# Optimization experiments

Hardware: AMD Instinct MI355X
Metric: run time of the kernel (lower is better)

## Reference

```python
import jax, jax.numpy as jnp
import numpy as np

MAX_DEG = 6


def neighbor_lookup(atoms, edges, maskvalue, include_self):
    # atoms: (B, A, F), edges: (B, A, D) with -1 padding
    B, A, F = atoms.shape
    D = edges.shape[-1]
    mask = edges >= 0
    idx = jnp.where(mask, edges, 0).reshape(B, A * D)
    g = jnp.take_along_axis(atoms, idx[:, :, None], axis=1).reshape(B, A, D, F)
    g = jnp.where(mask[..., None], g, maskvalue)
    if include_self:
        g = jnp.concatenate([atoms[:, :, None, :], g], axis=2)  # (B,A,D+1,F)
    return g


def graph_conv(atoms, bonds, edges, W, b):
    # W: (MAX_DEG, F_in+BF, C), b: (MAX_DEG, C)
    deg = (edges >= 0).sum(-1)  # (B, A)
    summed_atoms = neighbor_lookup(atoms, edges, 0.0, True).sum(2)  # self + neighbors
    summed_bonds = bonds.sum(2)
    feats = jnp.concatenate([summed_atoms, summed_bonds], axis=-1)
    out = jnp.zeros(feats.shape[:2] + (W.shape[-1],), feats.dtype)
    for d in range(MAX_DEG):  # small fixed loop over degrees
        h = jax.nn.relu(feats @ W[d] + b[d])
        out = out + jnp.where((deg == d)[..., None], h, 0.0)
    return out


def graph_pool(atoms, edges):
    g = neighbor_lookup(atoms, edges, -jnp.inf, True)  # self included -> finite max
    return g.max(axis=2)


def graph_output(atoms, bonds, edges, Wo, bo):
    deg = (edges >= 0).sum(-1)
    feats = jnp.concatenate([atoms, bonds.sum(2)], axis=-1)
    out = jax.nn.softmax(feats @ Wo + bo, axis=-1)
    mask = (deg != 0)[..., None]  # zero out padded atoms
    return jnp.where(mask, out, 0.0).sum(axis=1)  # (B, hid)


def setup_inputs():
    key = jax.random.key(0)
    ks = jax.random.split(key, 16)
    B, A, D = 4096, 64, 6
    AF, BF, H = 37, 6, 128
    s = lambda k, sh: (jax.random.normal(k, sh, jnp.float32) * 0.05)
    return {
        "atoms": jax.random.normal(ks[0], (B, A, AF), jnp.float32),
        "bonds": jax.random.normal(ks[1], (B, A, D, BF), jnp.float32),
        "edges": jax.random.randint(ks[2], (B, A, D), -1, A),
        "W1": s(ks[3], (MAX_DEG, AF + BF, H)),
        "b1": s(ks[4], (MAX_DEG, H)),
        "W2": s(ks[5], (MAX_DEG, H + BF, H)),
        "b2": s(ks[6], (MAX_DEG, H)),
        "Wo": s(ks[7], (H + BF, H)),
        "bo": s(ks[8], (H,)),
        "Wm1": s(ks[9], (H, H // 2)),
        "bm1": s(ks[10], (H // 2,)),
        "Wm2": s(ks[11], (H // 2, H // 4)),
        "bm2": s(ks[12], (H // 4,)),
        "Wm3": s(ks[13], (H // 4, 1)),
        "bm3": s(ks[14], (1,)),
    }


def reference(atoms, bonds, edges, W1, b1, W2, b2, Wo, bo, Wm1, bm1, Wm2, bm2, Wm3, bm3):
    x = graph_conv(atoms, bonds, edges, W1, b1)
    x = graph_pool(x, edges)
    x = graph_conv(x, bonds, edges, W2, b2)
    x = graph_pool(x, edges)
    fp = graph_output(x, bonds, edges, Wo, bo)
    h = jax.nn.relu(fp @ Wm1 + bm1)
    h = jax.nn.relu(h @ Wm2 + bm2)
    out = (h @ Wm3 + bm3).squeeze()  # (B,)
    return out
```

## Files before the change

kernel.cpp:

```cpp
#include <hip/hip_runtime.h>
#include <math.h>


__device__ __forceinline__ float4 max4(float4 a, float4 b) {
  return make_float4(fmaxf(a.x, b.x), fmaxf(a.y, b.y), fmaxf(a.z, b.z), fmaxf(a.w, b.w));
}

__device__ __forceinline__ float4 nbr_max(const float4* sx4, const int* se, int a, int c4) {
  float4 m = sx4[a * 32 + c4];
#pragma unroll
  for (int d = 0; d < 6; ++d) {
    int e = se[a * 6 + d];
    if (e >= 0) m = max4(m, sx4[e * 32 + c4]);
  }
  return m;
}

__device__ __forceinline__ float4 nbr_sum(const float4* sx4, const int* se, int a, int c4) {
  float4 s = sx4[a * 32 + c4];
#pragma unroll
  for (int d = 0; d < 6; ++d) {
    int e = se[a * 6 + d];
    if (e >= 0) {
      float4 v = sx4[e * 32 + c4];
      s.x += v.x; s.y += v.y; s.z += v.z; s.w += v.w;
    }
  }
  return s;
}

__device__ __forceinline__ float4 nbr_wmax(const float4* sx4, const int* se, const int* sdeg,
                                           int a, int c4) {
  float4 m = make_float4(0.f, 0.f, 0.f, 0.f);
  if (sdeg[a] < 6) m = max4(m, sx4[a * 32 + c4]);
#pragma unroll
  for (int d = 0; d < 6; ++d) {
    int e = se[a * 6 + d];
    if (e >= 0 && sdeg[e] < 6) m = max4(m, sx4[e * 32 + c4]);
  }
  return m;
}

__global__ __launch_bounds__(512, 8) void qsar_fused(
    const float* __restrict__ atoms, const float* __restrict__ bonds,
    const int* __restrict__ edges,
    const float* __restrict__ W1, const float* __restrict__ b1,
    const float* __restrict__ W2, const float* __restrict__ b2,
    const float* __restrict__ Wo, const float* __restrict__ bo,
    const float* __restrict__ Wm1, const float* __restrict__ bm1,
    const float* __restrict__ Wm2, const float* __restrict__ bm2,
    const float* __restrict__ Wm3, const float* __restrict__ bm3,
    float* __restrict__ out)
{
  const int b    = blockIdx.x;
  const int tid  = threadIdx.x;
  const int hid  = tid >> 5;
  const int hl   = tid & 31;

  __shared__ float s_x[64 * 128];
  __shared__ float s_sa[608];
  __shared__ float s_bsum[64 * 8];
  __shared__ int   s_edges[64 * 6];
  __shared__ int   s_deg[64];
  __shared__ int   s_work[64];
  __shared__ int   s_perm[64];
  __shared__ float s_rsum[64];
  __shared__ int   s_nwork, s_na, s_nz;

  float4* sx4  = reinterpret_cast<float4*>(s_x);
  float*  s_fp = s_sa;
  float*  s_h1 = s_sa + 512;
  float*  s_h2 = s_sa + 576;

  {
    const int* ge = edges + (size_t)b * (64 * 6);
    for (int i = tid; i < 64 * 6; i += 512) s_edges[i] = ge[i];
    const float* gb = bonds + (size_t)b * (64 * 36);
    for (int i = tid; i < 64 * 6; i += 512) {
      int a = i / 6, f = i - a * 6;
      float s = 0.f;
#pragma unroll
      for (int d = 0; d < 6; ++d) s += gb[a * 36 + d * 6 + f];
      s_bsum[a * 8 + f] = s;
    }
#pragma unroll
    for (int j = 0; j < 4; ++j) sx4[tid + j * 512] = make_float4(0.f, 0.f, 0.f, 0.f);
    if (tid == 0) { s_nwork = 0; s_na = 0; s_nz = 0; }
  }
  __syncthreads();

  if (tid < 64) {
    int dcnt = 0;
#pragma unroll
    for (int d = 0; d < 6; ++d) dcnt += (s_edges[tid * 6 + d] >= 0) ? 1 : 0;
    s_deg[tid] = dcnt;
    if (dcnt < 6) { int p = atomicAdd(&s_nwork, 1); s_work[p] = tid; }
  }
  __syncthreads();

  if (tid < 64) {
    int nzf = (s_deg[tid] < 6) ? 1 : 0;
#pragma unroll
    for (int d = 0; d < 6; ++d) {
      int e = s_edges[tid * 6 + d];
      if (e >= 0 && s_deg[e] < 6) nzf = 1;
    }
    if (nzf) { int p = atomicAdd(&s_na, 1); s_perm[p] = tid; }
    else     { int p = atomicAdd(&s_nz, 1); s_perm[63 - p] = tid; }
  }

  {
    const int nw = s_nwork;
    const float* ga = atoms + (size_t)b * (64 * 37);
    const int c0 = hl * 4;
    for (int cb = 0; cb < nw; cb += 16) {
      const int cnt = (nw - cb < 16) ? (nw - cb) : 16;
      for (int i = tid; i < cnt * 37; i += 512) {
        int wi = i / 37, k = i - wi * 37;
        int a = s_work[cb + wi];
        float f = ga[a * 37 + k];
#pragma unroll
        for (int d = 0; d < 6; ++d) {
          int e = s_edges[a * 6 + d];
          if (e >= 0) f += ga[e * 37 + k];
        }
        s_sa[wi * 38 + k] = f;
      }
      __syncthreads();
      for (int w = hid; w < cnt; w += 16) {
        const int a = s_work[cb + w];
        const int d = s_deg[a];
        const float4* wdf4 = reinterpret_cast<const float4*>(W1 + d * (43 * 128));
        float4 acc = *reinterpret_cast<const float4*>(&b1[d * 128 + c0]);
#pragma unroll 4
        for (int k = 0; k < 37; ++k) {
          const float ff = s_sa[w * 38 + k];
          const float4 w4 = wdf4[k * 32 + hl];
          acc.x = fmaf(ff, w4.x, acc.x); acc.y = fmaf(ff, w4.y, acc.y);
          acc.z = fmaf(ff, w4.z, acc.z); acc.w = fmaf(ff, w4.w, acc.w);
        }
#pragma unroll
        for (int kk = 0; kk < 6; ++kk) {
          const float ff = s_bsum[a * 8 + kk];
          const float4 w4 = wdf4[(37 + kk) * 32 + hl];
          acc.x = fmaf(ff, w4.x, acc.x); acc.y = fmaf(ff, w4.y, acc.y);
          acc.z = fmaf(ff, w4.z, acc.z); acc.w = fmaf(ff, w4.w, acc.w);
        }
        *reinterpret_cast<float4*>(&s_x[a * 128 + c0]) =
            make_float4(fmaxf(acc.x, 0.f), fmaxf(acc.y, 0.f),
                        fmaxf(acc.z, 0.f), fmaxf(acc.w, 0.f));
      }
      __syncthreads();
    }
  }
  __syncthreads();

  {
    float4 v0 = nbr_max(sx4, s_edges, (tid + 0 * 512) >> 5, tid & 31);
    float4 v1 = nbr_max(sx4, s_edges, (tid + 1 * 512) >> 5, tid & 31);
    float4 v2 = nbr_max(sx4, s_edges, (tid + 2 * 512) >> 5, tid & 31);
    float4 v3 = nbr_max(sx4, s_edges, (tid + 3 * 512) >> 5, tid & 31);
    __syncthreads();
    sx4[tid + 0 * 512] = v0; sx4[tid + 1 * 512] = v1;
    sx4[tid + 2 * 512] = v2; sx4[tid + 3 * 512] = v3;
  }
  __syncthreads();

  {
    const float4 z = make_float4(0.f, 0.f, 0.f, 0.f);
    float4 v0 = z, v1 = z, v2 = z, v3 = z;
    if (s_deg[(tid + 0 * 512) >> 5] < 6) v0 = nbr_sum(sx4, s_edges, (tid + 0 * 512) >> 5, tid & 31);
    if (s_deg[(tid + 1 * 512) >> 5] < 6) v1 = nbr_sum(sx4, s_edges, (tid + 1 * 512) >> 5, tid & 31);
    if (s_deg[(tid + 2 * 512) >> 5] < 6) v2 = nbr_sum(sx4, s_edges, (tid + 2 * 512) >> 5, tid & 31);
    if (s_deg[(tid + 3 * 512) >> 5] < 6) v3 = nbr_sum(sx4, s_edges, (tid + 3 * 512) >> 5, tid & 31);
    __syncthreads();
    if (s_deg[(tid + 0 * 512) >> 5] < 6) sx4[tid + 0 * 512] = v0;
    if (s_deg[(tid + 1 * 512) >> 5] < 6) sx4[tid + 1 * 512] = v1;
    if (s_deg[(tid + 2 * 512) >> 5] < 6) sx4[tid + 2 * 512] = v2;
    if (s_deg[(tid + 3 * 512) >> 5] < 6) sx4[tid + 3 * 512] = v3;
  }
  __syncthreads();

  {
    const int nw = s_nwork;
    const int c0 = hl * 4;
    for (int w = hid; w < nw; w += 16) {
      const int a = s_work[w];
      const int d = s_deg[a];
      const float4* wdf4 = reinterpret_cast<const float4*>(W2 + d * (134 * 128));
      float4 acc = *reinterpret_cast<const float4*>(&b2[d * 128 + c0]);
#pragma unroll 4
      for (int k = 0; k < 128; ++k) {
        const float ff = s_x[a * 128 + k];
        const float4 w4 = wdf4[k * 32 + hl];
        acc.x = fmaf(ff, w4.x, acc.x); acc.y = fmaf(ff, w4.y, acc.y);
        acc.z = fmaf(ff, w4.z, acc.z); acc.w = fmaf(ff, w4.w, acc.w);
      }
#pragma unroll
      for (int kk = 0; kk < 6; ++kk) {
        const float ff = s_bsum[a * 8 + kk];
        const float4 w4 = wdf4[(128 + kk) * 32 + hl];
        acc.x = fmaf(ff, w4.x, acc.x); acc.y = fmaf(ff, w4.y, acc.y);
        acc.z = fmaf(ff, w4.z, acc.z); acc.w = fmaf(ff, w4.w, acc.w);
      }
      *reinterpret_cast<float4*>(&s_x[a * 128 + c0]) =
          make_float4(fmaxf(acc.x, 0.f), fmaxf(acc.y, 0.f),
                      fmaxf(acc.z, 0.f), fmaxf(acc.w, 0.f));
    }
  }
  __syncthreads();

  {
    float4 v0 = nbr_wmax(sx4, s_edges, s_deg, (tid + 0 * 512) >> 5, tid & 31);
    float4 v1 = nbr_wmax(sx4, s_edges, s_deg, (tid + 1 * 512) >> 5, tid & 31);
    float4 v2 = nbr_wmax(sx4, s_edges, s_deg, (tid + 2 * 512) >> 5, tid & 31);
    float4 v3 = nbr_wmax(sx4, s_edges, s_deg, (tid + 3 * 512) >> 5, tid & 31);
    __syncthreads();
    sx4[tid + 0 * 512] = v0; sx4[tid + 1 * 512] = v1;
    sx4[tid + 2 * 512] = v2; sx4[tid + 3 * 512] = v3;
  }
  __syncthreads();

  {
    const int c0 = hl * 4;
    const int na = s_na;
    const int sl = hid * 4;
    const int at0 = s_perm[sl + 0], at1 = s_perm[sl + 1];
    const int at2 = s_perm[sl + 2], at3 = s_perm[sl + 3];
    float a00 = 0.f, a01 = 0.f, a02 = 0.f, a03 = 0.f;
    float a10 = 0.f, a11 = 0.f, a12 = 0.f, a13 = 0.f;
    float a20 = 0.f, a21 = 0.f, a22 = 0.f, a23 = 0.f;
    float a30 = 0.f, a31 = 0.f, a32 = 0.f, a33 = 0.f;
    const float4* Wof4 = reinterpret_cast<const float4*>(Wo);
    if (sl < na) {
#pragma unroll 4
      for (int k = 0; k < 128; ++k) {
        const float4 w4 = Wof4[k * 32 + hl];
        const float f0 = s_x[at0 * 128 + k], f1 = s_x[at1 * 128 + k];
        const float f2 = s_x[at2 * 128 + k], f3 = s_x[at3 * 128 + k];
        a00 = fmaf(f0, w4.x, a00); a01 = fmaf(f0, w4.y, a01);
        a02 = fmaf(f0, w4.z, a02); a03 = fmaf(f0, w4.w, a03);
        a10 = fmaf(f1, w4.x, a10); a11 = fmaf(f1, w4.y, a11);
        a12 = fmaf(f1, w4.z, a12); a13 = fmaf(f1, w4.w, a13);
        a20 = fmaf(f2, w4.x, a20); a21 = fmaf(f2, w4.y, a21);
        a22 = fmaf(f2, w4.z, a22); a23 = fmaf(f2, w4.w, a23);
        a30 = fmaf(f3, w4.x, a30); a31 = fmaf(f3, w4.y, a31);
        a32 = fmaf(f3, w4.z, a32); a33 = fmaf(f3, w4.w, a33);
      }
    }
#pragma unroll
    for (int kk = 0; kk < 6; ++kk) {
      const float4 w4 = Wof4[(128 + kk) * 32 + hl];
      const float f0 = s_bsum[at0 * 8 + kk], f1 = s_bsum[at1 * 8 + kk];
      const float f2 = s_bsum[at2 * 8 + kk], f3 = s_bsum[at3 * 8 + kk];
      a00 = fmaf(f0, w4.x, a00); a01 = fmaf(f0, w4.y, a01);
      a02 = fmaf(f0, w4.z, a02); a03 = fmaf(f0, w4.w, a03);
      a10 = fmaf(f1, w4.x, a10); a11 = fmaf(f1, w4.y, a11);
      a12 = fmaf(f1, w4.z, a12); a13 = fmaf(f1, w4.w, a13);
      a20 = fmaf(f2, w4.x, a20); a21 = fmaf(f2, w4.y, a21);
      a22 = fmaf(f2, w4.z, a22); a23 = fmaf(f2, w4.w, a23);
      a30 = fmaf(f3, w4.x, a30); a31 = fmaf(f3, w4.y, a31);
      a32 = fmaf(f3, w4.z, a32); a33 = fmaf(f3, w4.w, a33);
    }
    const float4 bo4 = *reinterpret_cast<const float4*>(bo + c0);
    *reinterpret_cast<float4*>(&s_x[at0 * 128 + c0]) =
        make_float4(a00 + bo4.x, a01 + bo4.y, a02 + bo4.z, a03 + bo4.w);
    *reinterpret_cast<float4*>(&s_x[at1 * 128 + c0]) =
        make_float4(a10 + bo4.x, a11 + bo4.y, a12 + bo4.z, a13 + bo4.w);
    *reinterpret_cast<float4*>(&s_x[at2 * 128 + c0]) =
        make_float4(a20 + bo4.x, a21 + bo4.y, a22 + bo4.z, a23 + bo4.w);
    *reinterpret_cast<float4*>(&s_x[at3 * 128 + c0]) =
        make_float4(a30 + bo4.x, a31 + bo4.y, a32 + bo4.z, a33 + bo4.w);
  }
  __syncthreads();

  {
    const int a = tid >> 3, q = tid & 7;
    float* base = &s_x[a * 128 + q * 16];
    const float4 v0 = *reinterpret_cast<const float4*>(base + ((0 + tid) & 3) * 4);
    const float4 v1 = *reinterpret_cast<const float4*>(base + ((1 + tid) & 3) * 4);
    const float4 v2 = *reinterpret_cast<const float4*>(base + ((2 + tid) & 3) * 4);
    const float4 v3 = *reinterpret_cast<const float4*>(base + ((3 + tid) & 3) * 4);
    float mx = fmaxf(fmaxf(fmaxf(v0.x, v0.y), fmaxf(v0.z, v0.w)),
                     fmaxf(fmaxf(v1.x, v1.y), fmaxf(v1.z, v1.w)));
    mx = fmaxf(mx, fmaxf(fmaxf(fmaxf(v2.x, v2.y), fmaxf(v2.z, v2.w)),
                         fmaxf(fmaxf(v3.x, v3.y), fmaxf(v3.z, v3.w))));
    mx = fmaxf(mx, __shfl_xor(mx, 1));
    mx = fmaxf(mx, __shfl_xor(mx, 2));
    mx = fmaxf(mx, __shfl_xor(mx, 4));
    float4 e0, e1, e2, e3;
    e0.x = __expf(v0.x - mx); e0.y = __expf(v0.y - mx); e0.z = __expf(v0.z - mx); e0.w = __expf(v0.w - mx);
    e1.x = __expf(v1.x - mx); e1.y = __expf(v1.y - mx); e1.z = __expf(v1.z - mx); e1.w = __expf(v1.w - mx);
    e2.x = __expf(v2.x - mx); e2.y = __expf(v2.y - mx); e2.z = __expf(v2.z - mx); e2.w = __expf(v2.w - mx);
    e3.x = __expf(v3.x - mx); e3.y = __expf(v3.y - mx); e3.z = __expf(v3.z - mx); e3.w = __expf(v3.w - mx);
    float sm = e0.x + e0.y + e0.z + e0.w;
    sm += e1.x + e1.y + e1.z + e1.w;
    sm += e2.x + e2.y + e2.z + e2.w;
    sm += e3.x + e3.y + e3.z + e3.w;
    *reinterpret_cast<float4*>(base + ((0 + tid) & 3) * 4) = e0;
    *reinterpret_cast<float4*>(base + ((1 + tid) & 3) * 4) = e1;
    *reinterpret_cast<float4*>(base + ((2 + tid) & 3) * 4) = e2;
    *reinterpret_cast<float4*>(base + ((3 + tid) & 3) * 4) = e3;
    sm += __shfl_xor(sm, 1);
    sm += __shfl_xor(sm, 2);
    sm += __shfl_xor(sm, 4);
    if (q == 0) s_rsum[a] = (s_deg[a] != 0) ? (1.f / sm) : 0.f;
  }
  __syncthreads();

  {
    const int c = tid & 127, quarter = tid >> 7;
    float s = 0.f;
    for (int a2 = quarter * 16; a2 < quarter * 16 + 16; ++a2)
      s = fmaf(s_x[a2 * 128 + c], s_rsum[a2], s);
    s_fp[quarter * 128 + c] = s;
  }
  __syncthreads();
  if (tid < 128) s_fp[tid] += s_fp[128 + tid] + s_fp[256 + tid] + s_fp[384 + tid];
  __syncthreads();

  if (tid < 64) {
    float acc = bm1[tid];
    for (int k = 0; k < 128; ++k) acc = fmaf(s_fp[k], Wm1[k * 64 + tid], acc);
    s_h1[tid] = fmaxf(acc, 0.f);
  }
  __syncthreads();
  if (tid < 32) {
    float acc = bm2[tid];
    for (int k = 0; k < 64; ++k) acc = fmaf(s_h1[k], Wm2[k * 32 + tid], acc);
    s_h2[tid] = fmaxf(acc, 0.f);
  }
  __syncthreads();
  if (tid < 64) {
    float p = (tid < 32) ? s_h2[tid] * Wm3[tid] : 0.f;
#pragma unroll
    for (int off = 32; off > 0; off >>= 1) p += __shfl_xor(p, off);
    if (tid == 0) out[b] = p + bm3[0];
  }
}

extern "C" void kernel_launch(void* const* d_in, const int* in_sizes, int n_in,
                              void* d_out, int out_size, void* d_ws, size_t ws_size,
                              hipStream_t stream) {
  const float* atoms = (const float*)d_in[0];
  const float* bonds = (const float*)d_in[1];
  const int*   edges = (const int*)d_in[2];
  const float* W1  = (const float*)d_in[3];
  const float* b1  = (const float*)d_in[4];
  const float* W2  = (const float*)d_in[5];
  const float* b2  = (const float*)d_in[6];
  const float* Wo  = (const float*)d_in[7];
  const float* bo  = (const float*)d_in[8];
  const float* Wm1 = (const float*)d_in[9];
  const float* bm1 = (const float*)d_in[10];
  const float* Wm2 = (const float*)d_in[11];
  const float* bm2 = (const float*)d_in[12];
  const float* Wm3 = (const float*)d_in[13];
  const float* bm3 = (const float*)d_in[14];
  float* out = (float*)d_out;

  const int B = out_size;
  qsar_fused<<<dim3(B), dim3(512), 0, stream>>>(
      atoms, bonds, edges, W1, b1, W2, b2, Wo, bo,
      Wm1, bm1, Wm2, bm2, Wm3, bm3, out);
}
```

Measured before the change: 238.9 us.

## Deduplicate atom rows by degree-<6 neighborhood mask before second pool and output GEMM

Each atom gets a 64-bit mask of the non-full-degree atoms in its self-plus-neighbor set. Atoms with identical nonzero masks share one representative row, so the weighted max pool and the 128x128 output matmul run only once per unique mask. The bond-sum and bias terms are then added per atom in a separate pass. This trades the former 4-atom register-blocked GEMM for a deduplicated single-row loop, plus a 64-iteration shuffle search and an extra sync and gather stage.

```diff
diff --git a/kernel.cpp b/kernel.cpp
--- a/kernel.cpp
+++ b/kernel.cpp
@@ -63,9 +63,10 @@
   __shared__ int   s_edges[64 * 6];
   __shared__ int   s_deg[64];
   __shared__ int   s_work[64];
-  __shared__ int   s_perm[64];
+  __shared__ int   s_urow[64];
+  __shared__ int   s_uniq[64];
   __shared__ float s_rsum[64];
-  __shared__ int   s_nwork, s_na, s_nz;
+  __shared__ int   s_nwork, s_nu;
 
   float4* sx4  = reinterpret_cast<float4*>(s_x);
   float*  s_fp = s_sa;
@@ -85,7 +86,7 @@
     }
 #pragma unroll
     for (int j = 0; j < 4; ++j) sx4[tid + j * 512] = make_float4(0.f, 0.f, 0.f, 0.f);
-    if (tid == 0) { s_nwork = 0; s_na = 0; s_nz = 0; }
+    if (tid == 0) { s_nwork = 0; s_nu = 0; }
   }
   __syncthreads();
 
@@ -99,14 +100,25 @@
   __syncthreads();
 
   if (tid < 64) {
-    int nzf = (s_deg[tid] < 6) ? 1 : 0;
+    unsigned int mlo = 0u, mhi = 0u;
+    if (s_deg[tid] < 6) { if (tid < 32) mlo |= 1u << tid; else mhi |= 1u << (tid - 32); }
 #pragma unroll
     for (int d = 0; d < 6; ++d) {
       int e = s_edges[tid * 6 + d];
-      if (e >= 0 && s_deg[e] < 6) nzf = 1;
-    }
-    if (nzf) { int p = atomicAdd(&s_na, 1); s_perm[p] = tid; }
-    else     { int p = atomicAdd(&s_nz, 1); s_perm[63 - p] = tid; }
+      if (e >= 0 && s_deg[e] < 6) { if (e < 32) mlo |= 1u << e; else mhi |= 1u << (e - 32); }
+    }
+    const bool nz = (mlo | mhi) != 0u;
+    int rep = tid;
+    for (int bb = 0; bb < 64; ++bb) {
+      const unsigned int blo = (unsigned int)__shfl((int)mlo, bb);
+      const unsigned int bhi = (unsigned int)__shfl((int)mhi, bb);
+      if (bb < tid && blo == mlo && bhi == mhi && rep == tid) rep = bb;
+    }
+    int u = -1;
+    if (nz && rep == tid) u = atomicAdd(&s_nu, 1);
+    const int urep = __shfl(u, rep);
+    s_urow[tid] = nz ? urep : -1;
+    if (u >= 0) s_uniq[u] = tid;
   }
 
   {
@@ -211,66 +223,58 @@
   __syncthreads();
 
   {
-    float4 v0 = nbr_wmax(sx4, s_edges, s_deg, (tid + 0 * 512) >> 5, tid & 31);
-    float4 v1 = nbr_wmax(sx4, s_edges, s_deg, (tid + 1 * 512) >> 5, tid & 31);
-    float4 v2 = nbr_wmax(sx4, s_edges, s_deg, (tid + 2 * 512) >> 5, tid & 31);
-    float4 v3 = nbr_wmax(sx4, s_edges, s_deg, (tid + 3 * 512) >> 5, tid & 31);
+    const int lim = s_nu * 32;
+    const float4 z = make_float4(0.f, 0.f, 0.f, 0.f);
+    float4 v0 = z, v1 = z, v2 = z, v3 = z;
+    const int i0 = tid, i1 = tid + 512, i2 = tid + 1024, i3 = tid + 1536;
+    if (i0 < lim) v0 = nbr_wmax(sx4, s_edges, s_deg, s_uniq[i0 >> 5], i0 & 31);
+    if (i1 < lim) v1 = nbr_wmax(sx4, s_edges, s_deg, s_uniq[i1 >> 5], i1 & 31);
+    if (i2 < lim) v2 = nbr_wmax(sx4, s_edges, s_deg, s_uniq[i2 >> 5], i2 & 31);
+    if (i3 < lim) v3 = nbr_wmax(sx4, s_edges, s_deg, s_uniq[i3 >> 5], i3 & 31);
     __syncthreads();
-    sx4[tid + 0 * 512] = v0; sx4[tid + 1 * 512] = v1;
-    sx4[tid + 2 * 512] = v2; sx4[tid + 3 * 512] = v3;
-  }
-  __syncthreads();
-
-  {
+    if (i0 < lim) sx4[s_uniq[i0 >> 5] * 32 + (i0 & 31)] = v0;
+    if (i1 < lim) sx4[s_uniq[i1 >> 5] * 32 + (i1 & 31)] = v1;
+    if (i2 < lim) sx4[s_uniq[i2 >> 5] * 32 + (i2 & 31)] = v2;
+    if (i3 < lim) sx4[s_uniq[i3 >> 5] * 32 + (i3 & 31)] = v3;
+  }
+  __syncthreads();
+
+  {
+    const int nu = s_nu;
     const int c0 = hl * 4;
-    const int na = s_na;
-    const int sl = hid * 4;
-    const int at0 = s_perm[sl + 0], at1 = s_perm[sl + 1];
-    const int at2 = s_perm[sl + 2], at3 = s_perm[sl + 3];
-    float a00 = 0.f, a01 = 0.f, a02 = 0.f, a03 = 0.f;
-    float a10 = 0.f, a11 = 0.f, a12 = 0.f, a13 = 0.f;
-    float a20 = 0.f, a21 = 0.f, a22 = 0.f, a23 = 0.f;
-    float a30 = 0.f, a31 = 0.f, a32 = 0.f, a33 = 0.f;
     const float4* Wof4 = reinterpret_cast<const float4*>(Wo);
-    if (sl < na) {
+    for (int w = hid; w < nu; w += 16) {
+      const int arow = s_uniq[w] * 128;
+      float4 acc = make_float4(0.f, 0.f, 0.f, 0.f);
 #pragma unroll 4
       for (int k = 0; k < 128; ++k) {
+        const float ff = s_x[arow + k];
         const float4 w4 = Wof4[k * 32 + hl];
-        const float f0 = s_x[at0 * 128 + k], f1 = s_x[at1 * 128 + k];
-        const float f2 = s_x[at2 * 128 + k], f3 = s_x[at3 * 128 + k];
-        a00 = fmaf(f0, w4.x, a00); a01 = fmaf(f0, w4.y, a01);
-        a02 = fmaf(f0, w4.z, a02); a03 = fmaf(f0, w4.w, a03);
-        a10 = fmaf(f1, w4.x, a10); a11 = fmaf(f1, w4.y, a11);
-        a12 = fmaf(f1, w4.z, a12); a13 = fmaf(f1, w4.w, a13);
-        a20 = fmaf(f2, w4.x, a20); a21 = fmaf(f2, w4.y, a21);
-        a22 = fmaf(f2, w4.z, a22); a23 = fmaf(f2, w4.w, a23);
-        a30 = fmaf(f3, w4.x, a30); a31 = fmaf(f3, w4.y, a31);
-        a32 = fmaf(f3, w4.z, a32); a33 = fmaf(f3, w4.w, a33);
-      }
-    }
-#pragma unroll
-    for (int kk = 0; kk < 6; ++kk) {
-      const float4 w4 = Wof4[(128 + kk) * 32 + hl];
-      const float f0 = s_bsum[at0 * 8 + kk], f1 = s_bsum[at1 * 8 + kk];
-      const float f2 = s_bsum[at2 * 8 + kk], f3 = s_bsum[at3 * 8 + kk];
-      a00 = fmaf(f0, w4.x, a00); a01 = fmaf(f0, w4.y, a01);
-      a02 = fmaf(f0, w4.z, a02); a03 = fmaf(f0, w4.w, a03);
-      a10 = fmaf(f1, w4.x, a10); a11 = fmaf(f1, w4.y, a11);
-      a12 = fmaf(f1, w4.z, a12); a13 = fmaf(f1, w4.w, a13);
-      a20 = fmaf(f2, w4.x, a20); a21 = fmaf(f2, w4.y, a21);
-      a22 = fmaf(f2, w4.z, a22); a23 = fmaf(f2, w4.w, a23);
-      a30 = fmaf(f3, w4.x, a30); a31 = fmaf(f3, w4.y, a31);
-      a32 = fmaf(f3, w4.z, a32); a33 = fmaf(f3, w4.w, a33);
-    }
-    const float4 bo4 = *reinterpret_cast<const float4*>(bo + c0);
-    *reinterpret_cast<float4*>(&s_x[at0 * 128 + c0]) =
-        make_float4(a00 + bo4.x, a01 + bo4.y, a02 + bo4.z, a03 + bo4.w);
-    *reinterpret_cast<float4*>(&s_x[at1 * 128 + c0]) =
-        make_float4(a10 + bo4.x, a11 + bo4.y, a12 + bo4.z, a13 + bo4.w);
-    *reinterpret_cast<float4*>(&s_x[at2 * 128 + c0]) =
-        make_float4(a20 + bo4.x, a21 + bo4.y, a22 + bo4.z, a23 + bo4.w);
-    *reinterpret_cast<float4*>(&s_x[at3 * 128 + c0]) =
-        make_float4(a30 + bo4.x, a31 + bo4.y, a32 + bo4.z, a33 + bo4.w);
+        acc.x = fmaf(ff, w4.x, acc.x); acc.y = fmaf(ff, w4.y, acc.y);
+        acc.z = fmaf(ff, w4.z, acc.z); acc.w = fmaf(ff, w4.w, acc.w);
+      }
+      *reinterpret_cast<float4*>(&s_x[arow + c0]) = acc;
+    }
+  }
+  __syncthreads();
+
+  {
+    float st[16];
+#pragma unroll
+    for (int j = 0; j < 16; ++j) {
+      const int e = tid + j * 512;
+      const int a = e >> 7, c = e & 127;
+      const int ur = s_urow[a];
+      float acc = bo[c];
+#pragma unroll
+      for (int kk = 0; kk < 6; ++kk)
+        acc = fmaf(s_bsum[a * 8 + kk], Wo[(128 + kk) * 128 + c], acc);
+      if (ur >= 0) acc += s_x[s_uniq[ur] * 128 + c];
+      st[j] = acc;
+    }
+    __syncthreads();
+#pragma unroll
+    for (int j = 0; j < 16; ++j) s_x[tid + j * 512] = st[j];
   }
   __syncthreads();
 
```

Measured after the change: 266.3 us. 1.12x slower.
